# Kernel optimization log

Measured on AMD Instinct MI355X. Metric: run time of the kernel, lower is better.

## Reference

```python
import jax, jax.numpy as jnp
import numpy as np

B, N, DIM = 4, 4096, 1024
HEADS, DIM_HEAD = 16, 64
ATTN_SCALE = 8.0
EPS = 1e-12


def setup_inputs() -> dict:
    key = jax.random.key(0)
    k1, k2, k3 = jax.random.split(key, 3)
    dim_inner = HEADS * DIM_HEAD
    return {
        "x": jax.random.normal(k1, (B, N, DIM), dtype=jnp.float32),
        "gamma": jnp.ones((DIM,), dtype=jnp.float32),
        "w_qkv": jax.random.normal(k2, (3 * dim_inner, DIM), dtype=jnp.float32) * 0.02,
        "temperature": jnp.ones((HEADS, 1, 1), dtype=jnp.float32),
        "w_out": jax.random.normal(k3, (DIM, dim_inner), dtype=jnp.float32) * 0.02,
    }


def _l2norm(t, axis=-1):
    # matches F.normalize: x / max(||x||, eps)
    n = jnp.sqrt(jnp.sum(t * t, axis=axis, keepdims=True))
    return t / jnp.maximum(n, EPS)


def reference(x, gamma, w_qkv, temperature, w_out):
    b, n, dim = x.shape
    h, dh = HEADS, DIM_HEAD
    # RMSNorm: F.normalize(x, dim=-1) * sqrt(dim) * gamma
    xn = _l2norm(x) * jnp.sqrt(jnp.float32(dim)) * gamma
    # QKV projection, rearrange 'b n (qkv h d) -> qkv b h d n'
    qkv = jnp.einsum('bnc,oc->bno', xn, w_qkv)
    qkv = qkv.reshape(b, n, 3, h, dh).transpose(2, 0, 3, 4, 1)  # (3, b, h, dh, n)
    q, k, v = qkv[0], qkv[1], qkv[2]
    # l2-normalize along n (last axis), learned per-head temperature on q
    q = _l2norm(q) * jnp.exp(temperature)
    k = _l2norm(k)
    # cross-covariance attention over feature dim: scores are (b,h,dh,dh)
    sim = jnp.einsum('bhdn,bhen->bhde', q, k) * ATTN_SCALE
    attn = jax.nn.softmax(sim, axis=-1)
    out = jnp.einsum('bhde,bhen->bhdn', attn, v)
    # rearrange 'b h d n -> b n (h d)' and output projection
    out = out.transpose(0, 3, 1, 2).reshape(b, n, h * dh)
    return jnp.einsum('bni,oi->bno', out, w_out)
```

## Files before the change

### kernel.cpp

```cpp
#include <hip/hip_runtime.h>
#include <hip/hip_bf16.h>
#include <cstdint>
#include <cstddef>

#define BB    4
#define NN    4096
#define DIM   1024
#define HEADS 16
#define DH    64
#define DIN   1024
#define NQO   3072
#define MTOT  (BB*NN)
#define KDIM  1024
#define EPS_F 1e-12f

using bf16 = __hip_bfloat16;
typedef __attribute__((ext_vector_type(8))) short bf16x8;
typedef __attribute__((ext_vector_type(4))) float f32x4;

__device__ __forceinline__ void gload_lds16(const void* g, void* l) {
    __builtin_amdgcn_global_load_lds(
        (const __attribute__((address_space(1))) void*)g,
        (__attribute__((address_space(3))) void*)l,
        16, 0, 0);
}

__device__ __forceinline__ ushort bf16_bits(float x) {
    union { bf16 h; ushort u; } c;
    c.h = __float2bfloat16(x);
    return c.u;
}

__device__ __forceinline__ float b2f(ushort u) {
    union { unsigned u32; float f; } c;
    c.u32 = ((unsigned)u) << 16;
    return c.f;
}

__global__ __launch_bounds__(256) void k_rmsnorm(const float* __restrict__ x,
                                                 const float* __restrict__ gamma,
                                                 bf16* __restrict__ xn) {
    int row = blockIdx.x;
    int t = threadIdx.x;
    const float4* xr = (const float4*)(x + (size_t)row * DIM);
    float4 v = xr[t];
    float ss = v.x * v.x + v.y * v.y + v.z * v.z + v.w * v.w;
#pragma unroll
    for (int off = 32; off; off >>= 1) ss += __shfl_down(ss, off, 64);
    __shared__ float red[4];
    int lane = t & 63, w = t >> 6;
    if (lane == 0) red[w] = ss;
    __syncthreads();
    float tot = red[0] + red[1] + red[2] + red[3];
    float scale = 32.0f / fmaxf(sqrtf(tot), EPS_F);
    float4 g = ((const float4*)gamma)[t];
    union { ushort4 u4; ushort us[4]; } o;
    o.us[0] = bf16_bits(v.x * scale * g.x);
    o.us[1] = bf16_bits(v.y * scale * g.y);
    o.us[2] = bf16_bits(v.z * scale * g.z);
    o.us[3] = bf16_bits(v.w * scale * g.w);
    ((ushort4*)(xn + (size_t)row * DIM))[t] = o.u4;
}

__global__ __launch_bounds__(256) void k_cast_bf16(const float* __restrict__ s,
                                                   bf16* __restrict__ d, int n4) {
    int i = blockIdx.x * blockDim.x + threadIdx.x;
    if (i >= n4) return;
    float4 v = ((const float4*)s)[i];
    union { ushort4 u4; ushort us[4]; } o;
    o.us[0] = bf16_bits(v.x); o.us[1] = bf16_bits(v.y);
    o.us[2] = bf16_bits(v.z); o.us[3] = bf16_bits(v.w);
    ((ushort4*)d)[i] = o.u4;
}

__global__ __launch_bounds__(256) void k_zero(float* __restrict__ p, int n) {
    int i = blockIdx.x * 256 + threadIdx.x;
    if (i < n) p[i] = 0.0f;
}

template<int MODE>
__global__ __launch_bounds__(512, 1) void k_gemm256(const bf16* __restrict__ A,
                                                    const bf16* __restrict__ W,
                                                    void* __restrict__ outp) {
    __shared__ short lds[65536];
    char* ldsb = (char*)lds;
    const int t = threadIdx.x, lane = t & 63, wv = t >> 6;
    const int wm = wv >> 2, wn = wv & 3;
    const int tm = blockIdx.y * 256;
    const int tn = blockIdx.x * 256;
    const int NT = KDIM / 64;

    const int rowst = wv * 8 + (lane >> 3);
    const int srcxor = (((lane & 7) ^ (lane >> 3)) << 4);
    const bf16* Asrc = A + (size_t)(tm + rowst) * KDIM;
    const bf16* Wsrc = W + (size_t)(tn + rowst) * KDIM;

#define STAGE(bufo_, kt_) do {                                                   \
    int k0_ = (kt_) * 64;                                                        \
    _Pragma("unroll")                                                            \
    for (int r_ = 0; r_ < 4; ++r_)                                               \
        gload_lds16((const char*)(Asrc + (size_t)r_ * 64 * KDIM + k0_) + srcxor, \
                    ldsb + (bufo_) + r_ * 8192 + wv * 1024);                     \
    _Pragma("unroll")                                                            \
    for (int r_ = 0; r_ < 4; ++r_)                                               \
        gload_lds16((const char*)(Wsrc + (size_t)r_ * 64 * KDIM + k0_) + srcxor, \
                    ldsb + (bufo_) + 32768 + r_ * 8192 + wv * 1024);             \
} while (0)

    const int rxor = (lane & 7) << 4;
    int aoff[2], boff[2];
#pragma unroll
    for (int ks = 0; ks < 2; ++ks) {
        int cb = (ks * 64 + ((lane >> 4) << 4)) ^ rxor;
        aoff[ks] = (wm * 128 + (lane & 15)) * 128 + cb;
        boff[ks] = 32768 + (wn * 64 + (lane & 15)) * 128 + cb;
    }

    f32x4 acc[8][4] = {};
    bf16x8 af[8][2], bfr[4][2];

    STAGE(0, 0);
    asm volatile("s_waitcnt vmcnt(0)" ::: "memory");
    __syncthreads();

    for (int kt = 0; kt < NT; ++kt) {
        const int bufo = (kt & 1) << 16;
#pragma unroll
        for (int mf = 0; mf < 4; ++mf)
#pragma unroll
            for (int ks = 0; ks < 2; ++ks)
                af[mf][ks] = *(const bf16x8*)(ldsb + bufo + aoff[ks] + mf * 2048);
#pragma unroll
        for (int nf = 0; nf < 2; ++nf)
#pragma unroll
            for (int ks = 0; ks < 2; ++ks)
                bfr[nf][ks] = *(const bf16x8*)(ldsb + bufo + boff[ks] + nf * 2048);
        if (kt + 1 < NT) STAGE(bufo ^ 65536, kt + 1);
        __builtin_amdgcn_s_barrier();
        __builtin_amdgcn_s_setprio(1);
#pragma unroll
        for (int ks = 0; ks < 2; ++ks)
#pragma unroll
            for (int mf = 0; mf < 4; ++mf)
#pragma unroll
                for (int nf = 0; nf < 2; ++nf)
                    acc[mf][nf] = __builtin_amdgcn_mfma_f32_16x16x32_bf16(af[mf][ks], bfr[nf][ks], acc[mf][nf], 0, 0, 0);
        __builtin_amdgcn_s_setprio(0);
        __builtin_amdgcn_s_barrier();
#pragma unroll
        for (int mf = 4; mf < 8; ++mf)
#pragma unroll
            for (int ks = 0; ks < 2; ++ks)
                af[mf][ks] = *(const bf16x8*)(ldsb + bufo + aoff[ks] + mf * 2048);
        __builtin_amdgcn_s_barrier();
        __builtin_amdgcn_s_setprio(1);
#pragma unroll
        for (int ks = 0; ks < 2; ++ks)
#pragma unroll
            for (int mf = 4; mf < 8; ++mf)
#pragma unroll
                for (int nf = 0; nf < 2; ++nf)
                    acc[mf][nf] = __builtin_amdgcn_mfma_f32_16x16x32_bf16(af[mf][ks], bfr[nf][ks], acc[mf][nf], 0, 0, 0);
        __builtin_amdgcn_s_setprio(0);
        __builtin_amdgcn_s_barrier();
#pragma unroll
        for (int nf = 2; nf < 4; ++nf)
#pragma unroll
            for (int ks = 0; ks < 2; ++ks)
                bfr[nf][ks] = *(const bf16x8*)(ldsb + bufo + boff[ks] + nf * 2048);
        __builtin_amdgcn_s_barrier();
        __builtin_amdgcn_s_setprio(1);
#pragma unroll
        for (int ks = 0; ks < 2; ++ks)
#pragma unroll
            for (int mf = 0; mf < 4; ++mf)
#pragma unroll
                for (int nf = 2; nf < 4; ++nf)
                    acc[mf][nf] = __builtin_amdgcn_mfma_f32_16x16x32_bf16(af[mf][ks], bfr[nf][ks], acc[mf][nf], 0, 0, 0);
        __builtin_amdgcn_s_setprio(0);
        __builtin_amdgcn_s_barrier();
        __builtin_amdgcn_s_setprio(1);
#pragma unroll
        for (int ks = 0; ks < 2; ++ks)
#pragma unroll
            for (int mf = 4; mf < 8; ++mf)
#pragma unroll
                for (int nf = 2; nf < 4; ++nf)
                    acc[mf][nf] = __builtin_amdgcn_mfma_f32_16x16x32_bf16(af[mf][ks], bfr[nf][ks], acc[mf][nf], 0, 0, 0);
        __builtin_amdgcn_s_setprio(0);
        if (kt + 1 < NT) asm volatile("s_waitcnt vmcnt(0)" ::: "memory");
        __builtin_amdgcn_s_barrier();
    }
#undef STAGE

    if (MODE == 0) {
        bf16* qkv = (bf16*)outp;
        const int b = tm >> 12;
        if (tn < 2048) {
#pragma unroll
            for (int mf = 0; mf < 8; ++mf) {
                int mg = tm + wm * 128 + mf * 16 + ((lane >> 4) << 2);
                int nseq = mg & (NN - 1);
#pragma unroll
                for (int nf = 0; nf < 4; ++nf) {
                    int o = tn + wn * 64 + nf * 16 + (lane & 15);
                    size_t row = (size_t)((o >> 10) * 4 + b) * 1024 + (o & 1023);
                    union { ushort4 u4; ushort us[4]; } pk;
#pragma unroll
                    for (int r = 0; r < 4; ++r) pk.us[r] = bf16_bits(acc[mf][nf][r]);
                    *(ushort4*)(qkv + row * NN + nseq) = pk.u4;
                }
            }
        } else {
            bf16* vT = qkv + (size_t)8192 * NN;
#pragma unroll
            for (int mf = 0; mf < 8; ++mf) {
                int mg = tm + wm * 128 + mf * 16 + ((lane >> 4) << 2);
                int nseq = mg & (NN - 1);
#pragma unroll
                for (int nf = 0; nf < 4; ++nf) {
                    int o = tn + wn * 64 + nf * 16 + (lane & 15);
                    int hd = o & 1023;
                    size_t base = ((size_t)(b * 16 + (hd >> 6)) * NN + nseq) * 64 + (hd & 63);
#pragma unroll
                    for (int r = 0; r < 4; ++r)
                        vT[base + (size_t)r * 64] = __float2bfloat16(acc[mf][nf][r]);
                }
            }
        }
    } else {
        float* out = (float*)outp;
#pragma unroll
        for (int mf = 0; mf < 8; ++mf) {
            int mg = tm + wm * 128 + mf * 16 + ((lane >> 4) << 2);
#pragma unroll
            for (int nf = 0; nf < 4; ++nf) {
                int o = tn + wn * 64 + nf * 16 + (lane & 15);
#pragma unroll
                for (int r = 0; r < 4; ++r)
                    out[(size_t)(mg + r) * DIN + o] = acc[mf][nf][r];
            }
        }
    }
}

__global__ __launch_bounds__(256) void k_sim(const bf16* __restrict__ qkv,
                                             float* __restrict__ part,
                                             float* __restrict__ ss) {
    __shared__ short Ks[2][8192];
    const int chunk = blockIdx.x;
    const int bh = blockIdx.y;
    const int t = threadIdx.x, lane = t & 63, w = t >> 6;
    const bf16* qb = qkv + (size_t)(bh * 64) * NN;
    const bf16* kb = qkv + (size_t)(4096 + bh * 64) * NN;
    const int n0b = chunk * 512;

#define SIM_STAGE(buf, nt) do {                                              \
    int n0_ = n0b + (nt) * 128;                                              \
    _Pragma("unroll")                                                        \
    for (int cc = 0; cc < 4; ++cc) {                                         \
        int row_ = cc * 16 + (t >> 4);                                       \
        int colb_ = ((t & 15) << 4) ^ ((row_ & 7) << 4);                     \
        gload_lds16(kb + (size_t)row_ * NN + n0_ + (colb_ >> 1),             \
                    &Ks[buf][cc * 2048 + w * 512]);                          \
    }                                                                        \
} while (0)

    f32x4 acc[4] = {};
    float ssq = 0.f, ssk = 0.f;

    SIM_STAGE(0, 0);
    __syncthreads();
    for (int nt = 0; nt < 4; ++nt) {
        if (nt < 3) SIM_STAGE((nt + 1) & 1, nt + 1);
        {
            const int buf = nt & 1;
            const int n0 = n0b + nt * 128;
            bf16x8 af[4];
#pragma unroll
            for (int ks = 0; ks < 4; ++ks) {
                af[ks] = *(const bf16x8*)(qb + (size_t)(w * 16 + (lane & 15)) * NN +
                                          n0 + ks * 32 + ((lane >> 4) << 3));
#pragma unroll
                for (int i = 0; i < 8; ++i) { float f = b2f((ushort)af[ks][i]); ssq += f * f; }
            }
#pragma unroll
            for (int j = 0; j < 4; ++j) {
                int e = j * 16 + (lane & 15);
#pragma unroll
                for (int ks = 0; ks < 4; ++ks) {
                    bf16x8 bfr = *(const bf16x8*)((const char*)&Ks[buf][0] + e * 256 +
                                  ((ks * 64 + ((lane >> 4) << 4)) ^ ((e & 7) << 4)));
                    if (j == w) {
#pragma unroll
                        for (int i = 0; i < 8; ++i) { float f = b2f((ushort)bfr[i]); ssk += f * f; }
                    }
                    acc[j] = __builtin_amdgcn_mfma_f32_16x16x32_bf16(af[ks], bfr, acc[j], 0, 0, 0);
                }
            }
        }
        __syncthreads();
    }
#undef SIM_STAGE

    float vq = ssq; vq += __shfl_xor(vq, 16, 64); vq += __shfl_xor(vq, 32, 64);
    if (lane < 16) atomicAdd(&ss[bh * 64 + w * 16 + lane], vq);
    float vk = ssk; vk += __shfl_xor(vk, 16, 64); vk += __shfl_xor(vk, 32, 64);
    if (lane < 16) atomicAdd(&ss[4096 + bh * 64 + w * 16 + lane], vk);

    float* pb = part + (size_t)(bh * 8 + chunk) * 4096;
#pragma unroll
    for (int j = 0; j < 4; ++j) {
        int e = j * 16 + (lane & 15);
#pragma unroll
        for (int r = 0; r < 4; ++r) {
            int d = w * 16 + ((lane >> 4) << 2) + r;
            pb[d * 64 + e] = acc[j][r];
        }
    }
}

__global__ __launch_bounds__(256) void k_softfin(const float* __restrict__ part,
                                                 const float* __restrict__ ss,
                                                 const float* __restrict__ temp,
                                                 bf16* __restrict__ attn) {
    int bh = blockIdx.x;
    int t = threadIdx.x, e = t & 63, w = t >> 6;
    float expT = __expf(temp[bh & (HEADS - 1)]);
    float ike = 8.0f * expT / fmaxf(sqrtf(ss[4096 + bh * 64 + e]), EPS_F);
    const float* pb = part + (size_t)bh * 8 * 4096;
#pragma unroll 2
    for (int dd = 0; dd < 16; ++dd) {
        int d = w * 16 + dd;
        float s = 0.f;
#pragma unroll
        for (int c = 0; c < 8; ++c) s += pb[c * 4096 + d * 64 + e];
        float invq = 1.0f / fmaxf(sqrtf(ss[bh * 64 + d]), EPS_F);
        float logit = s * ike * invq;
        float m = logit;
#pragma unroll
        for (int off = 32; off; off >>= 1) m = fmaxf(m, __shfl_xor(m, off, 64));
        float p = __expf(logit - m);
        float sum = p;
#pragma unroll
        for (int off = 32; off; off >>= 1) sum += __shfl_xor(sum, off, 64);
        attn[(size_t)bh * 4096 + d * 64 + e] = __float2bfloat16(p / sum);
    }
}

__global__ __launch_bounds__(256) void k_attnv(const bf16* __restrict__ qkv,
                                               const bf16* __restrict__ attn,
                                               bf16* __restrict__ A2) {
    const int nc = blockIdx.x;
    const int bh = blockIdx.y;
    const int t = threadIdx.x, lane = t & 63, w = t >> 6;
    const bf16* vT = qkv + (size_t)8192 * NN + (size_t)bh * NN * 64;
    const bf16* ab = attn + (size_t)bh * 4096;
    const int nbase = nc * 256 + w * 64;

    bf16x8 bfr[4][2];
#pragma unroll
    for (int df = 0; df < 4; ++df)
#pragma unroll
        for (int ks = 0; ks < 2; ++ks)
            bfr[df][ks] = *(const bf16x8*)(ab + (df * 16 + (lane & 15)) * 64 +
                                           ks * 32 + ((lane >> 4) << 3));

    f32x4 acc[4][4] = {};
#pragma unroll
    for (int nf = 0; nf < 4; ++nf) {
#pragma unroll
        for (int ks = 0; ks < 2; ++ks) {
            bf16x8 af = *(const bf16x8*)(vT + (size_t)(nbase + nf * 16 + (lane & 15)) * 64 +
                                         ks * 32 + ((lane >> 4) << 3));
#pragma unroll
            for (int df = 0; df < 4; ++df)
                acc[nf][df] = __builtin_amdgcn_mfma_f32_16x16x32_bf16(af, bfr[df][ks], acc[nf][df], 0, 0, 0);
        }
    }
    const int b = bh >> 4, h = bh & 15;
#pragma unroll
    for (int nf = 0; nf < 4; ++nf)
#pragma unroll
        for (int df = 0; df < 4; ++df)
#pragma unroll
            for (int r = 0; r < 4; ++r) {
                int n = nbase + nf * 16 + ((lane >> 4) << 2) + r;
                int d = df * 16 + (lane & 15);
                A2[(size_t)(b * NN + n) * DIN + h * 64 + d] = __float2bfloat16(acc[nf][df][r]);
            }
}

extern "C" void kernel_launch(void* const* d_in, const int* in_sizes, int n_in,
                              void* d_out, int out_size, void* d_ws, size_t ws_size,
                              hipStream_t stream) {
    const float* x      = (const float*)d_in[0];
    const float* gamma  = (const float*)d_in[1];
    const float* w_qkv  = (const float*)d_in[2];
    const float* temp   = (const float*)d_in[3];
    const float* w_out  = (const float*)d_in[4];
    float* out = (float*)d_out;

    char* ws = (char*)d_ws;
    bf16*  qkv    = (bf16*)ws;
    bf16*  xn     = (bf16*)(ws + 100663296);
    bf16*  wq_bf  = (bf16*)(ws + 134217728);
    bf16*  wo_bf  = (bf16*)(ws + 140509184);
    float* ss     = (float*)(ws + 142606336);
    float* part   = (float*)(ws + 142639104);
    bf16*  attnw  = (bf16*)(ws + 151027712);

    k_rmsnorm<<<MTOT, 256, 0, stream>>>(x, gamma, xn);
    k_cast_bf16<<<(NQO * KDIM / 4 + 255) / 256, 256, 0, stream>>>(w_qkv, wq_bf, NQO * KDIM / 4);
    k_cast_bf16<<<(DIN * KDIM / 4 + 255) / 256, 256, 0, stream>>>(w_out, wo_bf, DIN * KDIM / 4);
    k_zero<<<32, 256, 0, stream>>>(ss, 8192);
    k_gemm256<0><<<dim3(NQO / 256, MTOT / 256), 512, 0, stream>>>(xn, wq_bf, (void*)qkv);
    k_sim<<<dim3(8, 64), 256, 0, stream>>>(qkv, part, ss);
    k_softfin<<<64, 256, 0, stream>>>(part, ss, temp, attnw);
    bf16* A2 = xn;
    k_attnv<<<dim3(16, 64), 256, 0, stream>>>(qkv, attnw, A2);
    k_gemm256<1><<<dim3(DIN / 256, MTOT / 256), 512, 0, stream>>>(A2, wo_bf, (void*)out);
}
```

Measured before the change: 328.6 us.

## Fuse prologue kernels, swizzle GEMM tile order, stage QKV epilogue through LDS

Merges the rmsnorm, the two weight casts and the zeroing kernel into one launch, which removes three launch gaps. Remaps GEMM workgroup IDs so that consecutive IDs are spread in eight strided groups, changing which tiles run concurrently and how they share cache. The QKV GEMM epilogue now transposes the tile through swizzled LDS so that global stores become coalesced 16-byte writes, replacing the strided 8-byte and 2-byte scattered stores. This adds two barriers and LDS traffic to the epilogue.

```diff
diff --git a/kernel.cpp b/kernel.cpp
--- a/kernel.cpp
+++ b/kernel.cpp
@@ -37,45 +37,53 @@
     return c.f;
 }
 
-__global__ __launch_bounds__(256) void k_rmsnorm(const float* __restrict__ x,
-                                                 const float* __restrict__ gamma,
-                                                 bf16* __restrict__ xn) {
-    int row = blockIdx.x;
+__global__ __launch_bounds__(256) void k_prologue(const float* __restrict__ x,
+                                                  const float* __restrict__ gamma,
+                                                  bf16* __restrict__ xn,
+                                                  const float* __restrict__ wq,
+                                                  bf16* __restrict__ wq_bf,
+                                                  const float* __restrict__ wo,
+                                                  bf16* __restrict__ wo_bf,
+                                                  float* __restrict__ ss) {
+    int blk = blockIdx.x;
     int t = threadIdx.x;
-    const float4* xr = (const float4*)(x + (size_t)row * DIM);
-    float4 v = xr[t];
-    float ss = v.x * v.x + v.y * v.y + v.z * v.z + v.w * v.w;
-#pragma unroll
-    for (int off = 32; off; off >>= 1) ss += __shfl_down(ss, off, 64);
-    __shared__ float red[4];
-    int lane = t & 63, w = t >> 6;
-    if (lane == 0) red[w] = ss;
-    __syncthreads();
-    float tot = red[0] + red[1] + red[2] + red[3];
-    float scale = 32.0f / fmaxf(sqrtf(tot), EPS_F);
-    float4 g = ((const float4*)gamma)[t];
-    union { ushort4 u4; ushort us[4]; } o;
-    o.us[0] = bf16_bits(v.x * scale * g.x);
-    o.us[1] = bf16_bits(v.y * scale * g.y);
-    o.us[2] = bf16_bits(v.z * scale * g.z);
-    o.us[3] = bf16_bits(v.w * scale * g.w);
-    ((ushort4*)(xn + (size_t)row * DIM))[t] = o.u4;
-}
-
-__global__ __launch_bounds__(256) void k_cast_bf16(const float* __restrict__ s,
-                                                   bf16* __restrict__ d, int n4) {
-    int i = blockIdx.x * blockDim.x + threadIdx.x;
-    if (i >= n4) return;
-    float4 v = ((const float4*)s)[i];
-    union { ushort4 u4; ushort us[4]; } o;
-    o.us[0] = bf16_bits(v.x); o.us[1] = bf16_bits(v.y);
-    o.us[2] = bf16_bits(v.z); o.us[3] = bf16_bits(v.w);
-    ((ushort4*)d)[i] = o.u4;
-}
-
-__global__ __launch_bounds__(256) void k_zero(float* __restrict__ p, int n) {
-    int i = blockIdx.x * 256 + threadIdx.x;
-    if (i < n) p[i] = 0.0f;
+    if (blk < 16384) {
+        int row = blk;
+        const float4* xr = (const float4*)(x + (size_t)row * DIM);
+        float4 v = xr[t];
+        float s = v.x * v.x + v.y * v.y + v.z * v.z + v.w * v.w;
+#pragma unroll
+        for (int off = 32; off; off >>= 1) s += __shfl_down(s, off, 64);
+        __shared__ float red[4];
+        int lane = t & 63, w = t >> 6;
+        if (lane == 0) red[w] = s;
+        __syncthreads();
+        float tot = red[0] + red[1] + red[2] + red[3];
+        float scale = 32.0f / fmaxf(sqrtf(tot), EPS_F);
+        float4 g = ((const float4*)gamma)[t];
+        union { ushort4 u4; ushort us[4]; } o;
+        o.us[0] = bf16_bits(v.x * scale * g.x);
+        o.us[1] = bf16_bits(v.y * scale * g.y);
+        o.us[2] = bf16_bits(v.z * scale * g.z);
+        o.us[3] = bf16_bits(v.w * scale * g.w);
+        ((ushort4*)(xn + (size_t)row * DIM))[t] = o.u4;
+    } else if (blk < 19456) {
+        int i = (blk - 16384) * 256 + t;
+        float4 v = ((const float4*)wq)[i];
+        union { ushort4 u4; ushort us[4]; } o;
+        o.us[0] = bf16_bits(v.x); o.us[1] = bf16_bits(v.y);
+        o.us[2] = bf16_bits(v.z); o.us[3] = bf16_bits(v.w);
+        ((ushort4*)wq_bf)[i] = o.u4;
+    } else if (blk < 20480) {
+        int i = (blk - 19456) * 256 + t;
+        float4 v = ((const float4*)wo)[i];
+        union { ushort4 u4; ushort us[4]; } o;
+        o.us[0] = bf16_bits(v.x); o.us[1] = bf16_bits(v.y);
+        o.us[2] = bf16_bits(v.z); o.us[3] = bf16_bits(v.w);
+        ((ushort4*)wo_bf)[i] = o.u4;
+    } else {
+        ss[(blk - 20480) * 256 + t] = 0.0f;
+    }
 }
 
 template<int MODE>
@@ -86,8 +94,12 @@
     char* ldsb = (char*)lds;
     const int t = threadIdx.x, lane = t & 63, wv = t >> 6;
     const int wm = wv >> 2, wn = wv & 3;
-    const int tm = blockIdx.y * 256;
-    const int tn = blockIdx.x * 256;
+
+    const int nwg = gridDim.x * gridDim.y;
+    const int lid = blockIdx.y * gridDim.x + blockIdx.x;
+    const int wg = (lid & 7) * (nwg >> 3) + (lid >> 3);
+    const int tm = (wg / gridDim.x) * 256;
+    const int tn = (wg % gridDim.x) * 256;
     const int NT = KDIM / 64;
 
     const int rowst = wv * 8 + (lane >> 3);
@@ -193,40 +205,63 @@
     }
 #undef STAGE
 
-    if (MODE == 0) {
+    const int b = tm >> 12;
+    const int tm4 = tm & (NN - 1);
+    if (MODE == 0 && tn < 2048) {
         bf16* qkv = (bf16*)outp;
-        const int b = tm >> 12;
-        if (tn < 2048) {
-#pragma unroll
-            for (int mf = 0; mf < 8; ++mf) {
-                int mg = tm + wm * 128 + mf * 16 + ((lane >> 4) << 2);
-                int nseq = mg & (NN - 1);
-#pragma unroll
-                for (int nf = 0; nf < 4; ++nf) {
-                    int o = tn + wn * 64 + nf * 16 + (lane & 15);
-                    size_t row = (size_t)((o >> 10) * 4 + b) * 1024 + (o & 1023);
-                    union { ushort4 u4; ushort us[4]; } pk;
-#pragma unroll
-                    for (int r = 0; r < 4; ++r) pk.us[r] = bf16_bits(acc[mf][nf][r]);
-                    *(ushort4*)(qkv + row * NN + nseq) = pk.u4;
+        __syncthreads();
+#pragma unroll
+        for (int mf = 0; mf < 8; ++mf) {
+            int ml = wm * 128 + mf * 16 + ((lane >> 4) << 2);
+#pragma unroll
+            for (int nf = 0; nf < 4; ++nf) {
+                int ol = wn * 64 + nf * 16 + (lane & 15);
+                union { ushort us[4]; uint2 u2; } pk;
+#pragma unroll
+                for (int r = 0; r < 4; ++r) pk.us[r] = bf16_bits(acc[mf][nf][r]);
+                *(uint2*)(ldsb + ol * 512 + ((ml * 2) ^ ((ol & 31) << 4))) = pk.u2;
+            }
+        }
+        __syncthreads();
+        const int ol = t & 255, half = t >> 8;
+        int o = tn + ol;
+        size_t rowg = (size_t)((o >> 10) * 4 + b) * 1024 + (o & 1023);
+        bf16* dst = qkv + rowg * NN + tm4 + half * 128;
+        const int swz = (ol & 31) << 4;
+#pragma unroll
+        for (int i = 0; i < 16; ++i) {
+            int m0 = half * 128 + i * 8;
+            uint4 v = *(const uint4*)(ldsb + ol * 512 + ((m0 * 2) ^ swz));
+            *(uint4*)(dst + i * 8) = v;
+        }
+    } else if (MODE == 0) {
+        bf16* vT = (bf16*)outp + (size_t)8192 * NN;
+        __syncthreads();
+#pragma unroll
+        for (int mf = 0; mf < 8; ++mf) {
+            int mlb = wm * 128 + mf * 16 + ((lane >> 4) << 2);
+#pragma unroll
+            for (int nf = 0; nf < 4; ++nf) {
+                int ol = wn * 64 + nf * 16 + (lane & 15);
+#pragma unroll
+                for (int r = 0; r < 4; ++r) {
+                    int ml = mlb + r;
+                    *(ushort*)(ldsb + ml * 512 + ((ol * 2) ^ ((ml & 31) << 4))) =
+                        bf16_bits(acc[mf][nf][r]);
                 }
             }
-        } else {
-            bf16* vT = qkv + (size_t)8192 * NN;
-#pragma unroll
-            for (int mf = 0; mf < 8; ++mf) {
-                int mg = tm + wm * 128 + mf * 16 + ((lane >> 4) << 2);
-                int nseq = mg & (NN - 1);
-#pragma unroll
-                for (int nf = 0; nf < 4; ++nf) {
-                    int o = tn + wn * 64 + nf * 16 + (lane & 15);
-                    int hd = o & 1023;
-                    size_t base = ((size_t)(b * 16 + (hd >> 6)) * NN + nseq) * 64 + (hd & 63);
-#pragma unroll
-                    for (int r = 0; r < 4; ++r)
-                        vT[base + (size_t)r * 64] = __float2bfloat16(acc[mf][nf][r]);
-                }
-            }
+        }
+        __syncthreads();
+        const int ml = t & 255, half = t >> 8;
+        const int tnb = tn & 1023;
+        const int swz = (ml & 31) << 4;
+#pragma unroll
+        for (int i = 0; i < 16; ++i) {
+            int o0 = half * 128 + i * 8;
+            uint4 v = *(const uint4*)(ldsb + ml * 512 + ((o0 * 2) ^ swz));
+            int hd = tnb + o0;
+            bf16* dst = vT + ((size_t)(b * 16 + (hd >> 6)) * NN + tm4 + ml) * 64 + (hd & 63);
+            *(uint4*)dst = v;
         }
     } else {
         float* out = (float*)outp;
@@ -410,10 +445,7 @@
     float* part   = (float*)(ws + 142639104);
     bf16*  attnw  = (bf16*)(ws + 151027712);
 
-    k_rmsnorm<<<MTOT, 256, 0, stream>>>(x, gamma, xn);
-    k_cast_bf16<<<(NQO * KDIM / 4 + 255) / 256, 256, 0, stream>>>(w_qkv, wq_bf, NQO * KDIM / 4);
-    k_cast_bf16<<<(DIN * KDIM / 4 + 255) / 256, 256, 0, stream>>>(w_out, wo_bf, DIN * KDIM / 4);
-    k_zero<<<32, 256, 0, stream>>>(ss, 8192);
+    k_prologue<<<20512, 256, 0, stream>>>(x, gamma, xn, w_qkv, wq_bf, w_out, wo_bf, ss);
     k_gemm256<0><<<dim3(NQO / 256, MTOT / 256), 512, 0, stream>>>(xn, wq_bf, (void*)qkv);
     k_sim<<<dim3(8, 64), 256, 0, stream>>>(qkv, part, ss);
     k_softfin<<<64, 256, 0, stream>>>(part, ss, temp, attnw);
```

Measured after the change: 330.0 us. No clear change (+0.4%).
